# Kernel tuning notes

Hardware: AMD Instinct MI355X
Metric: run time of the kernel (lower is better)

## Reference

```python
import jax, jax.numpy as jnp
import numpy as np

N_E = 8192
E_DIM = 256
BETA = 0.25


def setup_inputs() -> dict:
    key = jax.random.key(0)
    k1, k2 = jax.random.split(key)
    z = jax.random.normal(k1, (16, 1024, E_DIM), dtype=jnp.float32)
    # matches embedding.weight.data.uniform_(-1/n_e, 1/n_e)
    embedding = jax.random.uniform(k2, (N_E, E_DIM), dtype=jnp.float32,
                                   minval=-1.0 / N_E, maxval=1.0 / N_E)
    return {"z": z, "embedding": embedding}


def reference(z, embedding):
    B, S, D = z.shape  # [16, 1024, 256]
    zf = z.reshape(-1, D)  # [N, D], N = B*S
    # squared L2 distances to every codebook entry: [N, n_e]
    d = (jnp.sum(zf * zf, axis=1, keepdims=True)
         + jnp.sum(embedding * embedding, axis=1)
         - 2.0 * (zf @ embedding.T))
    min_encoding_indices = jnp.argmin(d, axis=1)  # [N]
    # one-hot encodings (returned by the module) [N, n_e]
    min_encodings = jax.nn.one_hot(min_encoding_indices, N_E, dtype=jnp.float32)
    # z_q = min_encodings @ embedding == gather of nearest codes
    z_q = embedding[min_encoding_indices].reshape(z.shape)  # [B, S, D]
    sg = jax.lax.stop_gradient
    loss = jnp.mean((sg(z_q) - z) ** 2) + BETA * jnp.mean((z_q - sg(z)) ** 2)
    # straight-through estimator
    z_q_st = z + sg(z_q - z)
    e_mean = jnp.mean(min_encodings, axis=0)  # [n_e]
    perplexity = jnp.exp(-jnp.sum(e_mean * jnp.log(e_mean + 1e-10)))
    return (loss, z_q_st, perplexity, min_encodings, min_encoding_indices[:, None])
```

## Files before the change

kernel.cpp:

```cpp
#include <hip/hip_runtime.h>
#include <cstddef>

#define NROWS 16384
#define NE    8192
#define DD    256

typedef unsigned long long u64;
typedef float vf4 __attribute__((ext_vector_type(4)));
typedef short bf16x8 __attribute__((ext_vector_type(8)));
typedef float f32x4 __attribute__((ext_vector_type(4)));
typedef unsigned short us8 __attribute__((ext_vector_type(8)));

#define OH_TOT ((size_t)NROWS * NE)
#define OH_VEC ((OH_TOT - 4) / 4)
#define CAND_CAP 4000000
#define LLIST_CAP 2048

__global__ __launch_bounds__(256) void k_rowsq(
    const float* __restrict__ z, const float* __restrict__ emb,
    float* __restrict__ zsq, float* __restrict__ esq,
    u64* __restrict__ best, int* __restrict__ counts,
    float* __restrict__ wadd, int* __restrict__ cand_n,
    unsigned short* __restrict__ ebf)
{
  const int g = blockIdx.x * 256 + threadIdx.x;
  if (g == 0) *cand_n = 0;
  if (g < NE) counts[g] = 0;
  if (g < NROWS) best[g] = ~0ull;

  const float* row;
  float* outp;
  if (g < NROWS) { row = z + (size_t)g * DD;            outp = zsq + g; }
  else           { row = emb + (size_t)(g - NROWS) * DD; outp = esq + (g - NROWS); }

  float sa = 0.0f;
  float half_s[2];
#pragma unroll
  for (int h = 0; h < 2; ++h) {
    const float* p = row + h * 128;
    float r[8];
    {
      const float4 v0 = *(const float4*)(p);
      const float4 v1 = *(const float4*)(p + 4);
      const float xs[8] = {v0.x, v0.y, v0.z, v0.w, v1.x, v1.y, v1.z, v1.w};
#pragma unroll
      for (int j = 0; j < 8; ++j) {
        float sq = xs[j] * xs[j];
        asm volatile("" : "+v"(sq));
        r[j] = sq;
        sa += fabsf(xs[j]);
      }
    }
    for (int i = 8; i < 128; i += 8) {
      const float4 v0 = *(const float4*)(p + i);
      const float4 v1 = *(const float4*)(p + i + 4);
      const float xs[8] = {v0.x, v0.y, v0.z, v0.w, v1.x, v1.y, v1.z, v1.w};
#pragma unroll
      for (int j = 0; j < 8; ++j) {
        float sq = xs[j] * xs[j];
        asm volatile("" : "+v"(sq));
        r[j] = r[j] + sq;
        sa += fabsf(xs[j]);
      }
    }
    half_s[h] = ((r[0] + r[1]) + (r[2] + r[3])) + ((r[4] + r[5]) + (r[6] + r[7]));
  }
  const float zs = half_s[0] + half_s[1];
  *outp = zs;
  if (g < NROWS) {
    wadd[g] = 2.0f * ((zs + 2.0f) * 1.2e-7f + 2.0f * (1.0e-6f * sa) + 5.0e-8f);
  } else {
    const int c = g - NROWS;
    const int t = c >> 4, l = c & 15;
#pragma unroll
    for (int kt = 0; kt < 8; ++kt) {
#pragma unroll
      for (int kq = 0; kq < 4; ++kq) {
        const float4 v0 = *(const float4*)(row + kt * 32 + kq * 8);
        const float4 v1 = *(const float4*)(row + kt * 32 + kq * 8 + 4);
        const float xs[8] = {v0.x, v0.y, v0.z, v0.w, v1.x, v1.y, v1.z, v1.w};
        us8 u;
#pragma unroll
        for (int j = 0; j < 8; ++j) {
          const unsigned b = __float_as_uint(xs[j]);
          u[j] = (unsigned short)((b + 0x7FFFu + ((b >> 16) & 1u)) >> 16);
        }
        *(us8*)(ebf + (((size_t)(t * 8 + kt)) * 64 + kq * 16 + l) * 8) = u;
      }
    }
  }
}

__device__ __forceinline__ unsigned short f2bf_rne(float f) {
  const unsigned u = __float_as_uint(f);
  return (unsigned short)((u + 0x7FFFu + ((u >> 16) & 1u)) >> 16);
}
__device__ __forceinline__ unsigned encf(float f) {
  const unsigned u = __float_as_uint(f);
  return (u & 0x80000000u) ? ~u : (u | 0x80000000u);
}
__device__ __forceinline__ float decf(unsigned k) {
  const unsigned u = (k & 0x80000000u) ? (k ^ 0x80000000u) : ~k;
  return __uint_as_float(u);
}

__global__ __launch_bounds__(256)
__attribute__((amdgpu_waves_per_eu(3)))
void k_screen(
    const float* __restrict__ z, const unsigned short* __restrict__ ebf,
    const float* __restrict__ esq, const float* __restrict__ wadd,
    unsigned* __restrict__ cand, int* __restrict__ cand_n)
{
  __shared__ unsigned smin[64];
  __shared__ float wl[64];
  __shared__ unsigned llist[LLIST_CAP];
  __shared__ unsigned lcnt;
  __shared__ unsigned gbase;

  const int tid = threadIdx.x;
  const int b = blockIdx.x;
  const int x = b & 7;
  const int quarter = x >> 1;
  const int panel = (b >> 3) * 2 + (x & 1);
  const int R0 = panel * 64;
  const int C0 = quarter * 2048;
  const int T0 = C0 >> 4;

  const int wave = tid >> 6;
  const int lane = tid & 63;
  const int l15 = lane & 15;
  const int kg = lane >> 4;

  if (tid < 64) { smin[tid] = 0xFFFFFFFFu; wl[tid] = wadd[R0 + tid]; }
  if (tid == 0) lcnt = 0;

  bf16x8 af[8];
  {
    const float* zp_ = z + (size_t)(R0 + wave * 16 + l15) * DD + kg * 8;
#pragma unroll
    for (int kt = 0; kt < 8; ++kt) {
      const float4 a0 = *(const float4*)(zp_ + kt * 32);
      const float4 a1 = *(const float4*)(zp_ + kt * 32 + 4);
      bf16x8 w;
      w[0] = (short)f2bf_rne(a0.x); w[1] = (short)f2bf_rne(a0.y);
      w[2] = (short)f2bf_rne(a0.z); w[3] = (short)f2bf_rne(a0.w);
      w[4] = (short)f2bf_rne(a1.x); w[5] = (short)f2bf_rne(a1.y);
      w[6] = (short)f2bf_rne(a1.z); w[7] = (short)f2bf_rne(a1.w);
      af[kt] = w;
    }
  }
  __syncthreads();

  const int rbase = wave * 16 + kg * 4;
  const bf16x8* fb = (const bf16x8*)ebf;

  float rm[4] = {1e30f, 1e30f, 1e30f, 1e30f};
#pragma unroll 1
  for (int tt = 0; tt < 128; ++tt) {
    bf16x8 bfr[8];
#pragma unroll
    for (int kt = 0; kt < 8; ++kt)
      bfr[kt] = fb[(size_t)((T0 + tt) * 8 + kt) * 64 + lane];
    f32x4 e = (f32x4){0, 0, 0, 0}, o = (f32x4){0, 0, 0, 0};
#pragma unroll
    for (int kt = 0; kt < 8; kt += 2) {
      e = __builtin_amdgcn_mfma_f32_16x16x32_bf16(af[kt], bfr[kt], e, 0, 0, 0);
      o = __builtin_amdgcn_mfma_f32_16x16x32_bf16(af[kt + 1], bfr[kt + 1], o, 0, 0, 0);
    }
    const float ev = esq[C0 + tt * 16 + l15];
#pragma unroll
    for (int r = 0; r < 4; ++r)
      rm[r] = fminf(rm[r], ev - 2.0f * (e[r] + o[r]));
  }
#pragma unroll
  for (int r = 0; r < 4; ++r) {
    float mn = rm[r];
    mn = fminf(mn, __shfl_xor(mn, 1, 16));
    mn = fminf(mn, __shfl_xor(mn, 2, 16));
    mn = fminf(mn, __shfl_xor(mn, 4, 16));
    mn = fminf(mn, __shfl_xor(mn, 8, 16));
    if (l15 == 0) atomicMin(&smin[rbase + r], encf(mn));
  }
  __syncthreads();

  float thr[4];
#pragma unroll
  for (int r = 0; r < 4; ++r) thr[r] = decf(smin[rbase + r]) + wl[rbase + r];

#define PUSH(E_)                                                            \
  {                                                                         \
    const unsigned s_ = atomicAdd(&lcnt, 1u);                               \
    if (s_ < LLIST_CAP) llist[s_] = (E_);                                   \
    else { const int g_ = atomicAdd(cand_n, 1);                             \
           if (g_ < CAND_CAP) cand[g_] = (E_); }                            \
  }

#pragma unroll 1
  for (int tt = 0; tt < 128; ++tt) {
    bf16x8 bfr[8];
#pragma unroll
    for (int kt = 0; kt < 8; ++kt)
      bfr[kt] = fb[(size_t)((T0 + tt) * 8 + kt) * 64 + lane];
    f32x4 e = (f32x4){0, 0, 0, 0}, o = (f32x4){0, 0, 0, 0};
#pragma unroll
    for (int kt = 0; kt < 8; kt += 2) {
      e = __builtin_amdgcn_mfma_f32_16x16x32_bf16(af[kt], bfr[kt], e, 0, 0, 0);
      o = __builtin_amdgcn_mfma_f32_16x16x32_bf16(af[kt + 1], bfr[kt + 1], o, 0, 0, 0);
    }
    const int c = C0 + tt * 16 + l15;
    const float ev = esq[c];
    float rv[4];
    float gm = 1e30f;
#pragma unroll
    for (int r = 0; r < 4; ++r) {
      rv[r] = ev - 2.0f * (e[r] + o[r]);
      gm = fminf(gm, rv[r] - thr[r]);
    }
    if (gm <= 0.0f) {
#pragma unroll
      for (int r = 0; r < 4; ++r)
        if (rv[r] <= thr[r]) PUSH(((unsigned)(R0 + rbase + r) << 13) | (unsigned)c);
    }
  }

  __syncthreads();
  const unsigned n = (lcnt < LLIST_CAP) ? lcnt : LLIST_CAP;
  if (tid == 0) gbase = (unsigned)atomicAdd(cand_n, (int)n);
  __syncthreads();
  for (unsigned i = tid; i < n; i += 256) {
    const unsigned g = gbase + i;
    if (g < CAND_CAP) cand[g] = llist[i];
  }
}

__global__ __launch_bounds__(256) void k_zero(float* __restrict__ ohbase)
{
  const vf4 zz = {0.0f, 0.0f, 0.0f, 0.0f};
  float* zp = ohbase + 2;
  size_t s = (size_t)blockIdx.x * 16384 + threadIdx.x;
#pragma unroll 4
  for (int it = 0; it < 64; ++it) {
    if (s < OH_VEC) __builtin_nontemporal_store(zz, (vf4*)(zp + 4 * s));
    s += 256;
  }
  if (blockIdx.x == 0 && threadIdx.x == 0) {
    ohbase[0] = 0.0f; ohbase[1] = 0.0f;
    ohbase[OH_TOT - 2] = 0.0f; ohbase[OH_TOT - 1] = 0.0f;
  }
}

__global__ __launch_bounds__(256) void k_recheck(
    const float* __restrict__ z, const float* __restrict__ emb,
    const float* __restrict__ zsq, const float* __restrict__ esq,
    const unsigned* __restrict__ cand, const int* __restrict__ cand_n,
    u64* __restrict__ best)
{
  const int n = min(*cand_n, CAND_CAP);
  for (int i = blockIdx.x * 256 + threadIdx.x; i < n; i += gridDim.x * 256) {
    const unsigned e = cand[i];
    const int row = (int)(e >> 13);
    const int col = (int)(e & (NE - 1));
    const float4* zr = (const float4*)(z + (size_t)row * DD);
    const float4* er = (const float4*)(emb + (size_t)col * DD);
    float dot = 0.0f;
#pragma unroll 8
    for (int q = 0; q < 64; ++q) {
      const float4 a = zr[q];
      const float4 b = er[q];
      dot = fmaf(a.x, b.x, dot);
      dot = fmaf(a.y, b.y, dot);
      dot = fmaf(a.z, b.z, dot);
      dot = fmaf(a.w, b.w, dot);
    }
    const float s1 = zsq[row] + esq[col];
    const float dv = s1 - 2.0f * dot;
    atomicMin(&best[row], ((u64)__float_as_uint(dv) << 32) | (unsigned)col);
  }
}

__global__ __launch_bounds__(256) void k_gather2(
    const float* __restrict__ z, const float* __restrict__ emb,
    const u64* __restrict__ best,
    float* __restrict__ out_zq, float* __restrict__ out_onehot,
    float* __restrict__ out_idx, float* __restrict__ partials,
    int* __restrict__ counts)
{
  __shared__ float sred[256];
  const int row = blockIdx.x * 4 + (threadIdx.x >> 6);
  const int lane = threadIdx.x & 63;
  const int idx = (int)(unsigned)(best[row] & 0xffffffffull);
  const int k0 = lane * 4;

  const float4 e  = *(const float4*)(emb + (size_t)idx * DD + k0);
  const float4 zv = *(const float4*)(z + (size_t)row * DD + k0);
  *(float4*)(out_zq + (size_t)row * DD + k0) = e;

  const float dx = e.x - zv.x, dy = e.y - zv.y, dz = e.z - zv.z, dw = e.w - zv.w;
  sred[threadIdx.x] = dx * dx + dy * dy + dz * dz + dw * dw;

  if (lane == 0) {
    out_idx[row] = (float)idx;
    out_onehot[(size_t)row * NE + idx] = 1.0f;
    atomicAdd(&counts[idx], 1);
  }
  __syncthreads();
  for (int s = 128; s > 0; s >>= 1) {
    if (threadIdx.x < s) sred[threadIdx.x] += sred[threadIdx.x + s];
    __syncthreads();
  }
  if (threadIdx.x == 0) partials[blockIdx.x] = sred[0];
}

__global__ __launch_bounds__(256) void k_final(
    const int* __restrict__ counts, const float* __restrict__ partials,
    float* __restrict__ out_loss, float* __restrict__ out_perp)
{
  __shared__ float sred[256];
  __shared__ float sl[256];
  float le = 0.0f;
  for (int e = threadIdx.x; e < NE; e += 256) {
    const float p = (float)counts[e] * (1.0f / 16384.0f);
    le += p * logf(p + 1e-10f);
  }
  float ll = 0.0f;
  for (int b = threadIdx.x; b < NROWS / 4; b += 256) ll += partials[b];
  sred[threadIdx.x] = le;
  sl[threadIdx.x] = ll;
  __syncthreads();
  for (int s = 128; s > 0; s >>= 1) {
    if (threadIdx.x < s) {
      sred[threadIdx.x] += sred[threadIdx.x + s];
      sl[threadIdx.x] += sl[threadIdx.x + s];
    }
    __syncthreads();
  }
  if (threadIdx.x == 0) {
    *out_perp = expf(-sred[0]);
    *out_loss = sl[0] * (1.25f / 4194304.0f);
  }
}

extern "C" void kernel_launch(void* const* d_in, const int* in_sizes, int n_in,
                              void* d_out, int out_size, void* d_ws, size_t ws_size,
                              hipStream_t stream) {
  const float* z   = (const float*)d_in[0];
  const float* emb = (const float*)d_in[1];

  float* out        = (float*)d_out;
  float* out_loss   = out;
  float* out_zq     = out + 1;
  float* out_perp   = out + 4194305;
  float* out_onehot = out + 4194306;
  float* out_idx    = out + 138412034;

  float* zsq      = (float*)d_ws;
  float* esq      = zsq + NROWS;
  u64*   best     = (u64*)(esq + NE);
  int*   counts   = (int*)(best + NROWS);
  float* partials = (float*)(counts + NE);
  float* wadd     = partials + 4096;
  int*   cand_n   = (int*)(wadd + NROWS);
  unsigned short* ebf = (unsigned short*)(wadd + NROWS + 4);
  unsigned* cand  = (unsigned*)(ebf + (size_t)NE * DD);

  k_rowsq<<<96, 256, 0, stream>>>(z, emb, zsq, esq, best, counts, wadd, cand_n, ebf);
  k_screen<<<1024, 256, 0, stream>>>(z, ebf, esq, wadd, cand, cand_n);
  k_zero<<<2048, 256, 0, stream>>>(out_onehot);
  k_recheck<<<512, 256, 0, stream>>>(z, emb, zsq, esq, cand, cand_n, best);
  k_gather2<<<NROWS / 4, 256, 0, stream>>>(z, emb, best, out_zq, out_onehot,
                                           out_idx, partials, counts);
  k_final<<<1, 256, 0, stream>>>(counts, partials, out_loss, out_perp);
}
```

Measured before the change: 1.026 ms.

## Double per-wave row tile in screen kernel and fuse one-hot zeroing into it

The screen kernel now gives each block 128 rows by 1024 codebook columns instead of 64 by 2048, and each wave computes two 16-row MFMA tiles that share each loaded codebook fragment. This halves the codebook loads per MFMA. The separate one-hot zeroing kernel is folded into the tail of the screen kernel, which removes one launch and lets the store-bound zeroing overlap with compute from other blocks. In exchange, register pressure rises (the waves_per_eu hint is dropped), and the zeroing writes now sit on the screen kernel's critical path.

```diff
diff --git a/kernel.cpp b/kernel.cpp
--- a/kernel.cpp
+++ b/kernel.cpp
@@ -104,26 +104,24 @@
   return __uint_as_float(u);
 }
 
-__global__ __launch_bounds__(256)
-__attribute__((amdgpu_waves_per_eu(3)))
-void k_screen(
+__global__ __launch_bounds__(256) void k_screen(
     const float* __restrict__ z, const unsigned short* __restrict__ ebf,
     const float* __restrict__ esq, const float* __restrict__ wadd,
-    unsigned* __restrict__ cand, int* __restrict__ cand_n)
-{
-  __shared__ unsigned smin[64];
-  __shared__ float wl[64];
+    unsigned* __restrict__ cand, int* __restrict__ cand_n,
+    float* __restrict__ ohbase)
+{
+  __shared__ unsigned smin[128];
+  __shared__ float wl[128];
   __shared__ unsigned llist[LLIST_CAP];
   __shared__ unsigned lcnt;
   __shared__ unsigned gbase;
 
   const int tid = threadIdx.x;
   const int b = blockIdx.x;
-  const int x = b & 7;
-  const int quarter = x >> 1;
-  const int panel = (b >> 3) * 2 + (x & 1);
-  const int R0 = panel * 64;
-  const int C0 = quarter * 2048;
+  const int eighth = b & 7;
+  const int panel = b >> 3;
+  const int R0 = panel * 128;
+  const int C0 = eighth * 1024;
   const int T0 = C0 >> 4;
 
   const int wave = tid >> 6;
@@ -131,61 +129,83 @@
   const int l15 = lane & 15;
   const int kg = lane >> 4;
 
-  if (tid < 64) { smin[tid] = 0xFFFFFFFFu; wl[tid] = wadd[R0 + tid]; }
+  if (tid < 128) { smin[tid] = 0xFFFFFFFFu; wl[tid] = wadd[R0 + tid]; }
   if (tid == 0) lcnt = 0;
 
-  bf16x8 af[8];
+  bf16x8 af0[8], af1[8];
   {
-    const float* zp_ = z + (size_t)(R0 + wave * 16 + l15) * DD + kg * 8;
+    const float* zp0 = z + (size_t)(R0 + wave * 32 + l15) * DD + kg * 8;
+    const float* zp1 = zp0 + 16 * DD;
 #pragma unroll
     for (int kt = 0; kt < 8; ++kt) {
-      const float4 a0 = *(const float4*)(zp_ + kt * 32);
-      const float4 a1 = *(const float4*)(zp_ + kt * 32 + 4);
-      bf16x8 w;
+      const float4 a0 = *(const float4*)(zp0 + kt * 32);
+      const float4 a1 = *(const float4*)(zp0 + kt * 32 + 4);
+      const float4 c0 = *(const float4*)(zp1 + kt * 32);
+      const float4 c1 = *(const float4*)(zp1 + kt * 32 + 4);
+      bf16x8 w, v;
       w[0] = (short)f2bf_rne(a0.x); w[1] = (short)f2bf_rne(a0.y);
       w[2] = (short)f2bf_rne(a0.z); w[3] = (short)f2bf_rne(a0.w);
       w[4] = (short)f2bf_rne(a1.x); w[5] = (short)f2bf_rne(a1.y);
       w[6] = (short)f2bf_rne(a1.z); w[7] = (short)f2bf_rne(a1.w);
-      af[kt] = w;
-    }
-  }
-  __syncthreads();
-
-  const int rbase = wave * 16 + kg * 4;
+      v[0] = (short)f2bf_rne(c0.x); v[1] = (short)f2bf_rne(c0.y);
+      v[2] = (short)f2bf_rne(c0.z); v[3] = (short)f2bf_rne(c0.w);
+      v[4] = (short)f2bf_rne(c1.x); v[5] = (short)f2bf_rne(c1.y);
+      v[6] = (short)f2bf_rne(c1.z); v[7] = (short)f2bf_rne(c1.w);
+      af0[kt] = w;
+      af1[kt] = v;
+    }
+  }
+  __syncthreads();
+
+  const int rbase = wave * 32 + kg * 4;
   const bf16x8* fb = (const bf16x8*)ebf;
 
-  float rm[4] = {1e30f, 1e30f, 1e30f, 1e30f};
+  float rm[8];
+#pragma unroll
+  for (int i = 0; i < 8; ++i) rm[i] = 1e30f;
 #pragma unroll 1
-  for (int tt = 0; tt < 128; ++tt) {
+  for (int tt = 0; tt < 64; ++tt) {
     bf16x8 bfr[8];
 #pragma unroll
     for (int kt = 0; kt < 8; ++kt)
       bfr[kt] = fb[(size_t)((T0 + tt) * 8 + kt) * 64 + lane];
-    f32x4 e = (f32x4){0, 0, 0, 0}, o = (f32x4){0, 0, 0, 0};
+    f32x4 e0 = (f32x4){0, 0, 0, 0}, o0 = (f32x4){0, 0, 0, 0};
+    f32x4 e1 = (f32x4){0, 0, 0, 0}, o1 = (f32x4){0, 0, 0, 0};
 #pragma unroll
     for (int kt = 0; kt < 8; kt += 2) {
-      e = __builtin_amdgcn_mfma_f32_16x16x32_bf16(af[kt], bfr[kt], e, 0, 0, 0);
-      o = __builtin_amdgcn_mfma_f32_16x16x32_bf16(af[kt + 1], bfr[kt + 1], o, 0, 0, 0);
+      e0 = __builtin_amdgcn_mfma_f32_16x16x32_bf16(af0[kt], bfr[kt], e0, 0, 0, 0);
+      o0 = __builtin_amdgcn_mfma_f32_16x16x32_bf16(af0[kt + 1], bfr[kt + 1], o0, 0, 0, 0);
+      e1 = __builtin_amdgcn_mfma_f32_16x16x32_bf16(af1[kt], bfr[kt], e1, 0, 0, 0);
+      o1 = __builtin_amdgcn_mfma_f32_16x16x32_bf16(af1[kt + 1], bfr[kt + 1], o1, 0, 0, 0);
     }
     const float ev = esq[C0 + tt * 16 + l15];
 #pragma unroll
-    for (int r = 0; r < 4; ++r)
-      rm[r] = fminf(rm[r], ev - 2.0f * (e[r] + o[r]));
-  }
-#pragma unroll
-  for (int r = 0; r < 4; ++r) {
-    float mn = rm[r];
-    mn = fminf(mn, __shfl_xor(mn, 1, 16));
-    mn = fminf(mn, __shfl_xor(mn, 2, 16));
-    mn = fminf(mn, __shfl_xor(mn, 4, 16));
-    mn = fminf(mn, __shfl_xor(mn, 8, 16));
-    if (l15 == 0) atomicMin(&smin[rbase + r], encf(mn));
-  }
-  __syncthreads();
-
-  float thr[4];
-#pragma unroll
-  for (int r = 0; r < 4; ++r) thr[r] = decf(smin[rbase + r]) + wl[rbase + r];
+    for (int r = 0; r < 4; ++r) {
+      rm[r]     = fminf(rm[r],     ev - 2.0f * (e0[r] + o0[r]));
+      rm[4 + r] = fminf(rm[4 + r], ev - 2.0f * (e1[r] + o1[r]));
+    }
+  }
+#pragma unroll
+  for (int rs = 0; rs < 2; ++rs)
+#pragma unroll
+    for (int r = 0; r < 4; ++r) {
+      float mn = rm[rs * 4 + r];
+      mn = fminf(mn, __shfl_xor(mn, 1, 16));
+      mn = fminf(mn, __shfl_xor(mn, 2, 16));
+      mn = fminf(mn, __shfl_xor(mn, 4, 16));
+      mn = fminf(mn, __shfl_xor(mn, 8, 16));
+      if (l15 == 0) atomicMin(&smin[rbase + rs * 16 + r], encf(mn));
+    }
+  __syncthreads();
+
+  float thr[8];
+#pragma unroll
+  for (int rs = 0; rs < 2; ++rs)
+#pragma unroll
+    for (int r = 0; r < 4; ++r) {
+      const int R = rbase + rs * 16 + r;
+      thr[rs * 4 + r] = decf(smin[R]) + wl[R];
+    }
 
 #define PUSH(E_)                                                            \
   {                                                                         \
@@ -196,30 +216,38 @@
   }
 
 #pragma unroll 1
-  for (int tt = 0; tt < 128; ++tt) {
+  for (int tt = 0; tt < 64; ++tt) {
     bf16x8 bfr[8];
 #pragma unroll
     for (int kt = 0; kt < 8; ++kt)
       bfr[kt] = fb[(size_t)((T0 + tt) * 8 + kt) * 64 + lane];
-    f32x4 e = (f32x4){0, 0, 0, 0}, o = (f32x4){0, 0, 0, 0};
+    f32x4 e0 = (f32x4){0, 0, 0, 0}, o0 = (f32x4){0, 0, 0, 0};
+    f32x4 e1 = (f32x4){0, 0, 0, 0}, o1 = (f32x4){0, 0, 0, 0};
 #pragma unroll
     for (int kt = 0; kt < 8; kt += 2) {
-      e = __builtin_amdgcn_mfma_f32_16x16x32_bf16(af[kt], bfr[kt], e, 0, 0, 0);
-      o = __builtin_amdgcn_mfma_f32_16x16x32_bf16(af[kt + 1], bfr[kt + 1], o, 0, 0, 0);
+      e0 = __builtin_amdgcn_mfma_f32_16x16x32_bf16(af0[kt], bfr[kt], e0, 0, 0, 0);
+      o0 = __builtin_amdgcn_mfma_f32_16x16x32_bf16(af0[kt + 1], bfr[kt + 1], o0, 0, 0, 0);
+      e1 = __builtin_amdgcn_mfma_f32_16x16x32_bf16(af1[kt], bfr[kt], e1, 0, 0, 0);
+      o1 = __builtin_amdgcn_mfma_f32_16x16x32_bf16(af1[kt + 1], bfr[kt + 1], o1, 0, 0, 0);
     }
     const int c = C0 + tt * 16 + l15;
     const float ev = esq[c];
-    float rv[4];
+    float rv[8];
     float gm = 1e30f;
 #pragma unroll
     for (int r = 0; r < 4; ++r) {
-      rv[r] = ev - 2.0f * (e[r] + o[r]);
+      rv[r]     = ev - 2.0f * (e0[r] + o0[r]);
+      rv[4 + r] = ev - 2.0f * (e1[r] + o1[r]);
       gm = fminf(gm, rv[r] - thr[r]);
+      gm = fminf(gm, rv[4 + r] - thr[4 + r]);
     }
     if (gm <= 0.0f) {
 #pragma unroll
-      for (int r = 0; r < 4; ++r)
-        if (rv[r] <= thr[r]) PUSH(((unsigned)(R0 + rbase + r) << 13) | (unsigned)c);
+      for (int rs = 0; rs < 2; ++rs)
+#pragma unroll
+        for (int r = 0; r < 4; ++r)
+          if (rv[rs * 4 + r] <= thr[rs * 4 + r])
+            PUSH(((unsigned)(R0 + rbase + rs * 16 + r) << 13) | (unsigned)c);
     }
   }
 
@@ -231,21 +259,18 @@
     const unsigned g = gbase + i;
     if (g < CAND_CAP) cand[g] = llist[i];
   }
-}
-
-__global__ __launch_bounds__(256) void k_zero(float* __restrict__ ohbase)
-{
-  const vf4 zz = {0.0f, 0.0f, 0.0f, 0.0f};
-  float* zp = ohbase + 2;
-  size_t s = (size_t)blockIdx.x * 16384 + threadIdx.x;
+
+  {
+    const vf4 zz = {0.0f, 0.0f, 0.0f, 0.0f};
+    float* zp = ohbase + 2;
+    size_t zt = (size_t)b * 32768 + tid;
 #pragma unroll 4
-  for (int it = 0; it < 64; ++it) {
-    if (s < OH_VEC) __builtin_nontemporal_store(zz, (vf4*)(zp + 4 * s));
-    s += 256;
-  }
-  if (blockIdx.x == 0 && threadIdx.x == 0) {
-    ohbase[0] = 0.0f; ohbase[1] = 0.0f;
-    ohbase[OH_TOT - 2] = 0.0f; ohbase[OH_TOT - 1] = 0.0f;
+    for (int i = 0; i < 128; ++i) {
+      if (zt < OH_VEC) __builtin_nontemporal_store(zz, (vf4*)(zp + 4 * zt));
+      zt += 256;
+    }
+    if (b == 0 && tid == 0) { ohbase[0] = 0.0f; ohbase[1] = 0.0f; }
+    if (b == 1023 && tid == 0) { ohbase[OH_TOT - 2] = 0.0f; ohbase[OH_TOT - 1] = 0.0f; }
   }
 }
 
@@ -364,8 +389,7 @@
   unsigned* cand  = (unsigned*)(ebf + (size_t)NE * DD);
 
   k_rowsq<<<96, 256, 0, stream>>>(z, emb, zsq, esq, best, counts, wadd, cand_n, ebf);
-  k_screen<<<1024, 256, 0, stream>>>(z, ebf, esq, wadd, cand, cand_n);
-  k_zero<<<2048, 256, 0, stream>>>(out_onehot);
+  k_screen<<<1024, 256, 0, stream>>>(z, ebf, esq, wadd, cand, cand_n, out_onehot);
   k_recheck<<<512, 256, 0, stream>>>(z, emb, zsq, esq, cand, cand_n, best);
   k_gather2<<<NROWS / 4, 256, 0, stream>>>(z, emb, best, out_zq, out_onehot,
                                            out_idx, partials, counts);
```

New measurement: 975.8 us. -4.9%, faster.
